# Optimization experiments

Measured on AMD Instinct MI355X. Metric: run time of the kernel, lower is better.

Reference implementation:

```python
import jax, jax.numpy as jnp
import numpy as np

B, L, C_IN = 32, 244, 128
F_NUM, KS = 64, 5
HID = 512
SA_DIV = 3
F3 = F_NUM * 3
D_SA = F3 // SA_DIV  # must equal F_NUM (sa_div==3) for the view in SelfAttention


def setup_inputs() -> dict:
    key = jax.random.key(0)
    ks = jax.random.split(key, 16)

    def rn(k, shape, fan_in):
        return jax.random.normal(k, shape, dtype=jnp.float32) * float(np.sqrt(2.0 / fan_in))

    return {
        "x": jax.random.normal(ks[0], (B, L, C_IN), dtype=jnp.float32),
        "conv1_w": rn(ks[1], (F_NUM, 1, KS, 1), KS),
        "conv1_b": jnp.zeros((F_NUM,), jnp.float32),
        "conv2_w": rn(ks[2], (F_NUM, F_NUM, KS, 1), F_NUM * KS),
        "conv2_b": jnp.zeros((F_NUM,), jnp.float32),
        "conv3_w": rn(ks[3], (F_NUM, F_NUM, KS, 1), F_NUM * KS),
        "conv3_b": jnp.zeros((F_NUM,), jnp.float32),
        "conv4_w": rn(ks[4], (F_NUM, F_NUM, KS, 1), F_NUM * KS),
        "conv4_b": jnp.zeros((F_NUM,), jnp.float32),
        "wq": rn(ks[5], (D_SA, F3), F3),
        "wk": rn(ks[6], (D_SA, F3), F3),
        "wv": rn(ks[7], (D_SA, F3), F3),
        "wv1": rn(ks[8], (D_SA, F3), F3),
        "gamma": jnp.full((1,), 0.1, jnp.float32),
        "gru_wih": rn(ks[9], (3 * HID, F_NUM * C_IN), F_NUM * C_IN),
        "gru_whh": rn(ks[10], (3 * HID, HID), HID),
        "gru_bih": jnp.zeros((3 * HID,), jnp.float32),
        "gru_bhh": jnp.zeros((3 * HID,), jnp.float32),
        "fc_w": rn(ks[11], (1, HID), HID),
        "fc_b": jnp.zeros((1,), jnp.float32),
    }


def _conv2d(x, w, b):
    y = jax.lax.conv_general_dilated(
        x, w, window_strides=(1, 1), padding="VALID",
        dimension_numbers=("NCHW", "OIHW", "NCHW"))
    return y + b[None, :, None, None]


def reference(x, conv1_w, conv1_b, conv2_w, conv2_b, conv3_w, conv3_b, conv4_w, conv4_b,
              wq, wk, wv, wv1, gamma, gru_wih, gru_whh, gru_bih, gru_bhh, fc_w, fc_b):
    # conv stack: (B,1,L,C) -> (B,F,L',C), time dim shrinks by 4*(KS-1)
    h = x[:, None, :, :]
    h = jax.nn.relu(_conv2d(h, conv1_w, conv1_b))
    h = jax.nn.relu(_conv2d(h, conv2_w, conv2_b))
    h = jax.nn.relu(_conv2d(h, conv3_w, conv3_b))
    h = jax.nn.relu(_conv2d(h, conv4_w, conv4_b))
    Bn, Fn, Lp, Cn = h.shape
    step = int(np.ceil(Lp / 3))
    # static slice starts; last slice is x[:, :, -3:, :] (matches torch loop)
    starts = np.minimum(np.arange(step) * 3, Lp - 3)
    idx = starts[:, None] + np.arange(3)                               # (S,3)
    xs = h[:, :, idx, :]                                               # (B,F,S,3,C)
    xs = xs.transpose(0, 2, 1, 3, 4).reshape(Bn, step, Fn * 3, Cn)     # (B,S,F3,C)
    # batched SelfAttention (1x1 conv1d == matmul over channel dim)
    f = jnp.einsum("df,bsfc->bsdc", wq, xs)
    g = jnp.einsum("df,bsfc->bsdc", wk, xs)
    v = jnp.einsum("df,bsfc->bsdc", wv, xs)
    v1 = jnp.einsum("df,bsfc->bsdc", wv1, xs)
    # torch: softmax(bmm(f^T, g), dim=1) -> softmax over first C axis
    beta = jax.nn.softmax(jnp.einsum("bsdc,bsdk->bsck", f, g), axis=-2)
    o = gamma[0] * jnp.einsum("bsdc,bsck->bsdk", v, beta) + v1         # (B,S,F,C)
    seq = o.transpose(1, 0, 2, 3).reshape(step, Bn, Fn * Cn)           # (S,B,F*C)
    # single-layer GRU (PyTorch gate order r,z,n), seq-first
    xg = jnp.einsum("sbi,gi->sbg", seq, gru_wih) + gru_bih             # (S,B,3H)

    def gru_step(hprev, xg_t):
        hg = hprev @ gru_whh.T + gru_bhh
        xr, xz, xn = jnp.split(xg_t, 3, axis=-1)
        hr, hz, hn = jnp.split(hg, 3, axis=-1)
        r = jax.nn.sigmoid(xr + hr)
        z = jax.nn.sigmoid(xz + hz)
        n = jnp.tanh(xn + r * hn)
        hnew = (1.0 - z) * n + z * hprev
        return hnew, hnew

    h0 = jnp.zeros((Bn, HID), seq.dtype)
    _, outs = jax.lax.scan(gru_step, h0, xg)                            # (S,B,H)
    # temporal attention pooling over the time axis (axis 0)
    att = jnp.einsum("sbh,h->sb", outs, fc_w[0]) + fc_b[0]
    w_att = jax.nn.softmax(att, axis=0)[:, :, None]
    return jnp.sum(w_att * outs, axis=0)                                # (B,H)
```

## Files before the change

kernel.cpp:

```cpp
#include <hip/hip_runtime.h>
#include <math.h>


typedef __attribute__((ext_vector_type(8))) short short8;
typedef __attribute__((ext_vector_type(4))) float f32x4;

#define XG_STRIDE 3735552ull

__device__ inline float sigm(float x){ return 1.f/(1.f+__expf(-x)); }
__device__ inline unsigned short f2bf(float f){
    unsigned int u = __float_as_uint(f);
    u = (u + 0x7FFFu + ((u >> 16) & 1u)) >> 16;
    return (unsigned short)u;
}
__device__ inline float bf2f(unsigned short h){
    return __uint_as_float(((unsigned int)h) << 16);
}
__device__ inline int xcd_chunked(int orig, int nwg){
    int q = nwg >> 3, r = nwg & 7;
    int xcd = orig & 7, i = orig >> 3;
    return (xcd < r ? xcd*(q+1) : r*(q+1) + (xcd-r)*q) + i;
}

__global__ __launch_bounds__(256) void conv1_k(const float* __restrict__ x,
        unsigned short* __restrict__ out_h, unsigned short* __restrict__ out_l,
        const float* __restrict__ w1, const float* __restrict__ b1, int b_base)
{
    __shared__ float w1s[320];
    __shared__ float b1s[64];
    int t = threadIdx.x;
    for (int idx = t; idx < 320; idx += 256) w1s[idx] = w1[idx];
    if (t < 64)  b1s[t] = b1[t];
    __syncthreads();
    int i = blockIdx.x*256 + t;
    int c = i & 127; int t2 = i >> 7;
    int l = t2 % 240; int b = t2 / 240;
    const float* xp = x + ((size_t)(b_base + b)*244 + l)*128 + c;
    float xv[5];
    #pragma unroll
    for (int k=0;k<5;++k) xv[k] = xp[k*128];
    unsigned short* oh = out_h + (size_t)i*64;
    unsigned short* ol = out_l + (size_t)i*64;
    #pragma unroll
    for (int f8=0; f8<8; ++f8){
        unsigned short rh[8], rl[8];
        #pragma unroll
        for (int j=0;j<8;++j){
            int f = f8*8 + j;
            float a = b1s[f];
            #pragma unroll
            for (int k=0;k<5;++k) a += w1s[f*5+k]*xv[k];
            a = a > 0.f ? a : 0.f;
            unsigned short hi = f2bf(a);
            rh[j] = hi;
            rl[j] = f2bf(a - bf2f(hi));
        }
        *(short8*)(oh + f8*8) = *(short8*)rh;
        *(short8*)(ol + f8*8) = *(short8*)rl;
    }
}

__global__ __launch_bounds__(256) void repack_convw_k(const float* __restrict__ w2,
        const float* __restrict__ w3, const float* __restrict__ w4,
        unsigned short* __restrict__ wbf_h, unsigned short* __restrict__ wbf_l)
{
    int idx = blockIdx.x*256 + threadIdx.x;
    int fi = idx & 63; int t2 = idx >> 6;
    int fo = t2 & 63;  int t3 = t2 >> 6;
    int k = t3 % 5;    int layer = t3 / 5;
    const float* ws_ = (layer==0)? w2 : (layer==1)? w3 : w4;
    float v = ws_[(fo*64 + fi)*5 + k];
    unsigned short hi = f2bf(v);
    wbf_h[idx] = hi;
    wbf_l[idx] = f2bf(v - bf2f(hi));
}

__global__ __launch_bounds__(256) void conv_mfma_s(
        const unsigned short* __restrict__ in_h, const unsigned short* __restrict__ in_l,
        unsigned short* __restrict__ out_h, unsigned short* __restrict__ out_l,
        const unsigned short* __restrict__ wk_h, const unsigned short* __restrict__ wk_l,
        const float* __restrict__ bias, int Lin, int Lout)
{
    __shared__ __align__(16) unsigned short Abh[64*72], Abl[64*72];
    __shared__ __align__(16) unsigned short Wbh[64*72], Wbl[64*72];
    int nblk = gridDim.x;
    int lin = xcd_chunked(blockIdx.x, nblk);
    int ch = lin & 1; int rest = lin >> 1;
    int l = rest % Lout; int b = rest / Lout;

    int t = threadIdx.x;
    int lane = t & 63, w = t >> 6;
    int lr = lane & 15, lh = lane >> 4;
    f32x4 acc[4];
    #pragma unroll
    for (int nf=0;nf<4;++nf) acc[nf] = (f32x4)0.f;

    const size_t ib = ((size_t)b*Lin + l)*8192 + (size_t)ch*4096;
    for (int k=0;k<5;++k){
        __syncthreads();
        #pragma unroll
        for (int i=0;i<2;++i){
            int idx = i*256 + t; int row = idx>>3, c8 = idx&7;
            *(short8*)&Abh[row*72 + c8*8] = *(const short8*)(in_h + ib + (size_t)k*8192 + idx*8);
            *(short8*)&Abl[row*72 + c8*8] = *(const short8*)(in_l + ib + (size_t)k*8192 + idx*8);
        }
        #pragma unroll
        for (int i=0;i<2;++i){
            int idx = i*256 + t; int row = idx>>3, c8 = idx&7;
            *(short8*)&Wbh[row*72 + c8*8] = *(const short8*)(wk_h + k*4096 + idx*8);
            *(short8*)&Wbl[row*72 + c8*8] = *(const short8*)(wk_l + k*4096 + idx*8);
        }
        __syncthreads();
        #pragma unroll
        for (int kk=0;kk<2;++kk){
            short8 ah, al, bh[4], blo[4];
            ah = *(const short8*)&Abh[(w*16+lr)*72 + kk*32 + lh*8];
            al = *(const short8*)&Abl[(w*16+lr)*72 + kk*32 + lh*8];
            #pragma unroll
            for (int nf=0;nf<4;++nf){
                bh[nf]  = *(const short8*)&Wbh[(nf*16+lr)*72 + kk*32 + lh*8];
                blo[nf] = *(const short8*)&Wbl[(nf*16+lr)*72 + kk*32 + lh*8];
            }
            #pragma unroll
            for (int nf=0;nf<4;++nf){
                acc[nf] = __builtin_amdgcn_mfma_f32_16x16x32_bf16(ah, bh[nf],  acc[nf], 0,0,0);
                acc[nf] = __builtin_amdgcn_mfma_f32_16x16x32_bf16(ah, blo[nf], acc[nf], 0,0,0);
                acc[nf] = __builtin_amdgcn_mfma_f32_16x16x32_bf16(al, bh[nf],  acc[nf], 0,0,0);
            }
        }
    }
    const size_t ob = ((size_t)b*Lout + l)*8192;
    #pragma unroll
    for (int nf=0;nf<4;++nf){
        int fo = nf*16 + lr;
        float bv = bias[fo];
        #pragma unroll
        for (int q=0;q<4;++q){
            int c = ch*64 + w*16 + lh*4 + q;
            float v = acc[nf][q] + bv;
            v = v > 0.f ? v : 0.f;
            unsigned short hi = f2bf(v);
            out_h[ob + c*64 + fo] = hi;
            out_l[ob + c*64 + fo] = f2bf(v - bf2f(hi));
        }
    }
}

__global__ __launch_bounds__(256) void repack_wrep_k(const float* __restrict__ wq,
        const float* __restrict__ wk, const float* __restrict__ wv,
        const float* __restrict__ wv1,
        unsigned short* __restrict__ wr_h, unsigned short* __restrict__ wr_l)
{
    int idx = blockIdx.x*256 + threadIdx.x;
    int ko = idx % 192; int md = idx / 192;
    int m = md >> 6, d = md & 63;
    int jj = ko >> 6, f = ko & 63;
    const float* src = (m==0)? wq : (m==1)? wk : (m==2)? wv : wv1;
    float v = src[d*192 + f*3 + jj];
    unsigned short hi = f2bf(v);
    wr_h[idx] = hi;
    wr_l[idx] = f2bf(v - bf2f(hi));
}

__global__ __launch_bounds__(256) void project_mfma_s(
        const unsigned short* __restrict__ h_h, const unsigned short* __restrict__ h_l,
        const unsigned short* __restrict__ wr_h, const unsigned short* __restrict__ wr_l,
        float* __restrict__ Fo, float* __restrict__ Go,
        float* __restrict__ Vo, float* __restrict__ V1o)
{
    __shared__ __align__(16) unsigned short Abh[64*72], Abl[64*72];
    __shared__ __align__(16) unsigned short Bbh[64*72], Bbl[64*72];
    int nblk = gridDim.x;
    int lin = xcd_chunked(blockIdx.x, nblk);
    int z = lin & 7; int rest = lin >> 3;
    int s = rest % 76; int bl = rest / 76;
    int mz = z >> 1, mh = z & 1;

    int t = threadIdx.x;
    int lane = t & 63, w = t >> 6;
    int wm = w >> 1, wn = w & 1;
    int lr = lane & 15, lh = lane >> 4;
    f32x4 acc[2][2];
    #pragma unroll
    for (int mf=0;mf<2;++mf)
        #pragma unroll
        for (int nf=0;nf<2;++nf) acc[mf][nf] = (f32x4)0.f;

    for (int jj=0;jj<3;++jj){
        __syncthreads();
        const size_t ao_ = ((size_t)bl*228 + 3*s + jj)*8192 + (size_t)mh*4096;
        #pragma unroll
        for (int i=0;i<2;++i){
            int idx = i*256 + t; int row = idx>>3, c8 = idx&7;
            *(short8*)&Abh[row*72 + c8*8] = *(const short8*)(h_h + ao_ + idx*8);
            *(short8*)&Abl[row*72 + c8*8] = *(const short8*)(h_l + ao_ + idx*8);
        }
        #pragma unroll
        for (int i=0;i<2;++i){
            int idx = i*256 + t; int row = idx>>3, c8 = idx&7;
            size_t wo = (size_t)(mz*64 + row)*192 + jj*64 + c8*8;
            *(short8*)&Bbh[row*72 + c8*8] = *(const short8*)(wr_h + wo);
            *(short8*)&Bbl[row*72 + c8*8] = *(const short8*)(wr_l + wo);
        }
        __syncthreads();
        #pragma unroll
        for (int kk=0;kk<2;++kk){
            short8 ah[2], al[2], bh[2], blo[2];
            #pragma unroll
            for (int mf=0;mf<2;++mf){
                ah[mf] = *(const short8*)&Abh[(wm*32+mf*16+lr)*72 + kk*32 + lh*8];
                al[mf] = *(const short8*)&Abl[(wm*32+mf*16+lr)*72 + kk*32 + lh*8];
            }
            #pragma unroll
            for (int nf=0;nf<2;++nf){
                bh[nf]  = *(const short8*)&Bbh[(wn*32+nf*16+lr)*72 + kk*32 + lh*8];
                blo[nf] = *(const short8*)&Bbl[(wn*32+nf*16+lr)*72 + kk*32 + lh*8];
            }
            #pragma unroll
            for (int mf=0;mf<2;++mf)
                #pragma unroll
                for (int nf=0;nf<2;++nf){
                    acc[mf][nf] = __builtin_amdgcn_mfma_f32_16x16x32_bf16(ah[mf], bh[nf],  acc[mf][nf], 0,0,0);
                    acc[mf][nf] = __builtin_amdgcn_mfma_f32_16x16x32_bf16(ah[mf], blo[nf], acc[mf][nf], 0,0,0);
                    acc[mf][nf] = __builtin_amdgcn_mfma_f32_16x16x32_bf16(al[mf], bh[nf],  acc[mf][nf], 0,0,0);
                }
        }
    }
    float* dst = (mz==0)? Fo : (mz==1)? Go : (mz==2)? Vo : V1o;
    size_t bs = (size_t)bl*76 + s;
    #pragma unroll
    for (int mf=0;mf<2;++mf)
        #pragma unroll
        for (int nf=0;nf<2;++nf){
            int d = wn*32 + nf*16 + lr;
            int c0 = mh*64 + wm*32 + mf*16 + lh*4;
            *(f32x4*)&dst[(bs*64 + d)*128 + c0] = acc[mf][nf];
        }
}

__global__ __launch_bounds__(256) void attend_k(const float* __restrict__ Fg,
        const float* __restrict__ Gg, const float* __restrict__ Vg,
        const float* __restrict__ V1g, const float* __restrict__ gamma,
        unsigned short* __restrict__ seq_bf, int b_base)
{
    __shared__ float sm[16384];
    int t = threadIdx.x;
    int s = blockIdx.x, bl = blockIdx.y;
    size_t base = ((size_t)bl*76 + s)*8192;
    for (int i=t; i<8192; i+=256) sm[i]      = Fg[base+i];
    for (int i=t; i<8192; i+=256) sm[8192+i] = Gg[base+i];
    __syncthreads();

    int k = t & 127, ch = t >> 7;
    float sc[64];
    #pragma unroll
    for (int j=0;j<64;++j) sc[j]=0.f;
    for (int d=0; d<64; ++d){
        float gk = sm[8192 + d*128 + k];
        #pragma unroll
        for (int cj=0; cj<16; ++cj){
            float4 f4 = *(const float4*)&sm[d*128 + ch*64 + cj*4];
            sc[cj*4+0] += f4.x*gk; sc[cj*4+1] += f4.y*gk;
            sc[cj*4+2] += f4.z*gk; sc[cj*4+3] += f4.w*gk;
        }
    }
    __syncthreads();
    float m = -1e30f;
    #pragma unroll
    for (int j=0;j<64;++j) m = fmaxf(m, sc[j]);
    sm[t] = m;
    for (int i=t; i<8192; i+=256) sm[8192+i] = Vg[base+i];
    __syncthreads();
    m = fmaxf(sm[k], sm[128+k]);
    float lsum = 0.f;
    #pragma unroll
    for (int j=0;j<64;++j){ sc[j] = __expf(sc[j]-m); lsum += sc[j]; }
    __syncthreads();
    sm[t] = lsum;
    __syncthreads();
    float rinv = 1.f/(sm[k] + sm[128+k]);
    #pragma unroll
    for (int j=0;j<64;++j) sc[j] *= rinv;
    __syncthreads();

    if (ch == 0){
        #pragma unroll
        for (int j=0;j<64;++j) sm[j*128 + k] = sc[j];
    }
    __syncthreads();

    int k2 = t & 31, dq = t >> 5;
    float ao[8][4];
    #pragma unroll
    for (int j=0;j<8;++j)
        #pragma unroll
        for (int mm=0;mm<4;++mm) ao[j][mm]=0.f;

    for (int c2=0; c2<64; ++c2){
        float bv0 = sm[c2*128 + k2],    bv1 = sm[c2*128 + k2+32];
        float bv2 = sm[c2*128 + k2+64], bv3 = sm[c2*128 + k2+96];
        #pragma unroll
        for (int j=0;j<8;++j){
            float v = sm[8192 + (dq*8+j)*128 + c2];
            ao[j][0]+=v*bv0; ao[j][1]+=v*bv1; ao[j][2]+=v*bv2; ao[j][3]+=v*bv3;
        }
    }
    __syncthreads();
    if (ch == 1){
        #pragma unroll
        for (int j=0;j<64;++j) sm[j*128 + k] = sc[j];
    }
    __syncthreads();
    for (int c2=64; c2<128; ++c2){
        float bv0 = sm[(c2-64)*128 + k2],    bv1 = sm[(c2-64)*128 + k2+32];
        float bv2 = sm[(c2-64)*128 + k2+64], bv3 = sm[(c2-64)*128 + k2+96];
        #pragma unroll
        for (int j=0;j<8;++j){
            float v = sm[8192 + (dq*8+j)*128 + c2];
            ao[j][0]+=v*bv0; ao[j][1]+=v*bv1; ao[j][2]+=v*bv2; ao[j][3]+=v*bv3;
        }
    }

    float gm = gamma[0];
    size_t sbase = (size_t)(s*32 + b_base + bl)*8192;
    #pragma unroll
    for (int j=0;j<8;++j){
        int d = dq*8+j;
        #pragma unroll
        for (int mm=0;mm<4;++mm){
            int kk = k2 + 32*mm;
            float val = gm*ao[j][mm] + V1g[base + (size_t)d*128 + kk];
            seq_bf[sbase + (size_t)d*128 + kk] = f2bf(val);
        }
    }
}

__global__ __launch_bounds__(256) void conv_wih_bf16(const float* __restrict__ w,
        unsigned short* __restrict__ o)
{
    int i = (blockIdx.x*256 + threadIdx.x)*4;
    float4 v = *(const float4*)&w[i];
    ushort4 r;
    r.x = f2bf(v.x); r.y = f2bf(v.y); r.z = f2bf(v.z); r.w = f2bf(v.w);
    *(ushort4*)&o[i] = r;
}

__global__ __launch_bounds__(512) void gemm_xg_mfma(const unsigned short* __restrict__ A,
        const unsigned short* __restrict__ Bw, const float* __restrict__ bih,
        float* __restrict__ out, int nsplit)
{
    __shared__ float AsF[128*36];
    __shared__ float BsF[128*36];
    int nwg = 228*nsplit;
    int wgid = xcd_chunked(blockIdx.x, nwg);
    int kz = wgid / 228;
    int r2 = wgid % 228;
    int n0 = (r2 % 12) * 128, m0 = (r2 / 12) * 128;
    int klen = 8192 / nsplit;
    int kbase = kz * klen;
    int nkt = klen >> 6;

    int t = threadIdx.x;
    int w = t >> 6;
    int wm = w >> 1, wn = w & 1;
    int lane = t & 63, lr = lane & 15, lh = lane >> 4;

    f32x4 acc[2][4];
    #pragma unroll
    for (int mi=0;mi<2;++mi)
        #pragma unroll
        for (int ni=0;ni<4;++ni) acc[mi][ni] = (f32x4)0.f;

    float4 ra[2], rb[2];
    #pragma unroll
    for (int i=0;i<2;++i){
        int idx = i*512 + t; int row = idx>>3, seg = idx&7;
        ra[i] = *(const float4*)(A  + (size_t)(m0 + row)*8192 + kbase + seg*8);
        rb[i] = *(const float4*)(Bw + (size_t)(n0 + row)*8192 + kbase + seg*8);
    }
    for (int kt=0; kt<nkt; ++kt){
        __syncthreads();
        #pragma unroll
        for (int i=0;i<2;++i){
            int idx = i*512 + t; int row = idx>>3, seg = idx&7;
            *(float4*)&AsF[row*36 + seg*4] = ra[i];
            *(float4*)&BsF[row*36 + seg*4] = rb[i];
        }
        __syncthreads();
        if (kt < nkt-1){
            int k0 = kbase + (kt+1)*64;
            #pragma unroll
            for (int i=0;i<2;++i){
                int idx = i*512 + t; int row = idx>>3, seg = idx&7;
                ra[i] = *(const float4*)(A  + (size_t)(m0 + row)*8192 + k0 + seg*8);
                rb[i] = *(const float4*)(Bw + (size_t)(n0 + row)*8192 + k0 + seg*8);
            }
        }
        #pragma unroll
        for (int kk=0;kk<2;++kk){
            short8 af[2], bf_[4];
            #pragma unroll
            for (int mi=0;mi<2;++mi)
                af[mi] = *(short8*)&AsF[(wm*32 + mi*16 + lr)*36 + kk*16 + lh*4];
            #pragma unroll
            for (int ni=0;ni<4;++ni)
                bf_[ni] = *(short8*)&BsF[(wn*64 + ni*16 + lr)*36 + kk*16 + lh*4];
            #pragma unroll
            for (int mi=0;mi<2;++mi)
                #pragma unroll
                for (int ni=0;ni<4;++ni)
                    acc[mi][ni] = __builtin_amdgcn_mfma_f32_16x16x32_bf16(
                                      bf_[ni], af[mi], acc[mi][ni], 0, 0, 0);
        }
    }
    float* op = out + (size_t)kz*XG_STRIDE;
    #pragma unroll
    for (int ni=0;ni<4;++ni){
        int nbase = n0 + wn*64 + ni*16 + lh*4;
        float4 bi4 = (kz == 0) ? *(const float4*)&bih[nbase]
                               : make_float4(0.f,0.f,0.f,0.f);
        #pragma unroll
        for (int mi=0;mi<2;++mi){
            int m = m0 + wm*32 + mi*16 + lr;
            float4 o;
            o.x = acc[mi][ni][0] + bi4.x;
            o.y = acc[mi][ni][1] + bi4.y;
            o.z = acc[mi][ni][2] + bi4.z;
            o.w = acc[mi][ni][3] + bi4.w;
            *(float4*)&op[(size_t)m*1536 + nbase] = o;
        }
    }
}

__global__ __launch_bounds__(256) void build_whhp_k(const float* __restrict__ whh,
        float4* __restrict__ whh_p)
{
    int idx = blockIdx.x*256 + threadIdx.x;
    int i = idx >> 9, j = idx & 511;
    float4 o;
    o.x = whh[(size_t)j*512 + i];
    o.y = whh[(size_t)(512+j)*512 + i];
    o.z = whh[(size_t)(1024+j)*512 + i];
    o.w = 0.f;
    whh_p[idx] = o;
}

__global__ __launch_bounds__(1024) void gru_step_k(const float4* __restrict__ whh_p,
        const float* __restrict__ xg, const float* __restrict__ bhh,
        float* __restrict__ outs, int s, int nsplit)
{
    __shared__ float hl[2048];
    __shared__ float red[4][4][64][3];
    int t = threadIdx.x;
    int jc = blockIdx.x & 7, bq = blockIdx.x >> 3;
    for (int idx=t; idx<2048; idx+=1024)
        hl[idx] = outs[(size_t)s*16384 + (size_t)(bq*4 + (idx>>9))*512 + (idx&511)];
    __syncthreads();
    int jl = t & 63, bl = (t >> 6) & 3, iq = t >> 8;
    int j = jc*64 + jl;
    float a0=0.f,a1=0.f,a2=0.f;
    const float4* wp = whh_p + (size_t)(iq*128)*512 + j;
    const float* hb = hl + bl*512 + iq*128;
    #pragma unroll 4
    for (int i=0;i<128;++i){
        float4 w4 = wp[(size_t)i*512];
        float hv = hb[i];
        a0 += w4.x*hv; a1 += w4.y*hv; a2 += w4.z*hv;
    }
    red[iq][bl][jl][0] = a0; red[iq][bl][jl][1] = a1; red[iq][bl][jl][2] = a2;
    __syncthreads();
    if (t < 256){
        int jl2 = t & 63, bl2 = t >> 6;
        int j2 = jc*64 + jl2, b = bq*4 + bl2;
        float hr=0.f, hz=0.f, hn=0.f;
        #pragma unroll
        for (int q=0;q<4;++q){
            hr += red[q][bl2][jl2][0];
            hz += red[q][bl2][jl2][1];
            hn += red[q][bl2][jl2][2];
        }
        size_t xi = (size_t)(s*32 + b)*1536 + j2;
        float xr = xg[xi], xz = xg[xi+512], xn = xg[xi+1024];
        #pragma unroll 1
        for (int q2=1; q2<nsplit; ++q2){
            xr += xg[xi + (size_t)q2*XG_STRIDE];
            xz += xg[xi + 512 + (size_t)q2*XG_STRIDE];
            xn += xg[xi + 1024 + (size_t)q2*XG_STRIDE];
        }
        hr += bhh[j2]; hz += bhh[512+j2]; hn += bhh[1024+j2];
        float r = sigm(xr+hr), z = sigm(xz+hz);
        float n = tanhf(xn + r*hn);
        float hp = hl[bl2*512 + j2];
        float hnew = (1.f - z)*n + z*hp;
        outs[(size_t)(s+1)*16384 + (size_t)b*512 + j2] = hnew;
    }
}

__global__ __launch_bounds__(256) void pool_k(const float* __restrict__ outs,
        const float* __restrict__ fcw, const float* __restrict__ fcb,
        float* __restrict__ out)
{
    __shared__ float att[80], watt[128];
    int b = blockIdx.x, t = threadIdx.x;
    int w = t >> 6, lane = t & 63;
    for (int s = w; s < 76; s += 4){
        float acc = 0.f;
        const float* op = outs + (size_t)(s+1)*16384 + (size_t)b*512;
        #pragma unroll
        for (int hh = 0; hh < 512; hh += 64) acc += op[hh+lane]*fcw[hh+lane];
        #pragma unroll
        for (int off=32; off; off>>=1) acc += __shfl_down(acc, off);
        if (lane==0) att[s] = acc + fcb[0];
    }
    __syncthreads();
    if (t < 64){
        float a0 = (t<76)? att[t] : -1e30f;
        float a1 = (t+64<76)? att[t+64] : -1e30f;
        float m = fmaxf(a0,a1);
        #pragma unroll
        for (int off=32; off; off>>=1) m = fmaxf(m, __shfl_xor(m, off));
        float e0 = (t<76)? __expf(a0-m) : 0.f;
        float e1 = (t+64<76)? __expf(a1-m) : 0.f;
        float ssum = e0+e1;
        #pragma unroll
        for (int off=32; off; off>>=1) ssum += __shfl_xor(ssum, off);
        float ri = 1.f/ssum;
        watt[t] = e0*ri;
        watt[t+64] = e1*ri;
    }
    __syncthreads();
    for (int h = t; h < 512; h += 256){
        float acc=0.f;
        for (int s=0;s<76;++s) acc += watt[s]*outs[(size_t)(s+1)*16384 + (size_t)b*512 + h];
        out[(size_t)b*512 + h] = acc;
    }
}

extern "C" void kernel_launch(void* const* d_in, const int* in_sizes, int n_in,
                              void* d_out, int out_size, void* d_ws, size_t ws_size,
                              hipStream_t stream)
{
    const float* x   = (const float*)d_in[0];
    const float* w1  = (const float*)d_in[1];  const float* b1  = (const float*)d_in[2];
    const float* w2  = (const float*)d_in[3];  const float* b2  = (const float*)d_in[4];
    const float* w3  = (const float*)d_in[5];  const float* b3  = (const float*)d_in[6];
    const float* w4  = (const float*)d_in[7];  const float* b4  = (const float*)d_in[8];
    const float* wq  = (const float*)d_in[9];  const float* wk  = (const float*)d_in[10];
    const float* wv  = (const float*)d_in[11]; const float* wv1 = (const float*)d_in[12];
    const float* gamma = (const float*)d_in[13];
    const float* wih = (const float*)d_in[14]; const float* whh = (const float*)d_in[15];
    const float* bih = (const float*)d_in[16]; const float* bhh = (const float*)d_in[17];
    const float* fcw = (const float*)d_in[18]; const float* fcb = (const float*)d_in[19];

    int nb = 2, ns = 1;
    {
        auto need = [](int nb_, int ns_)->size_t{
            return ((size_t)nb_*4521984ull + 16117760ull
                    + (size_t)(ns_-1)*3735552ull)*4ull + 4096ull;
        };
        if      (ws_size >= need(8,4)){ nb = 8; ns = 4; }
        else if (ws_size >= need(8,2)){ nb = 8; ns = 2; }
        else if (ws_size >= need(4,2)){ nb = 4; ns = 2; }
        else if (ws_size >= need(2,2)){ nb = 2; ns = 2; }
    }

    float* ws = (float*)d_ws;
    size_t off = 0;
    size_t szAh = (size_t)nb*983040ull;
    size_t szBh = (size_t)nb*966656ull;
    size_t szP  = (size_t)nb*622592ull;
    unsigned short* bufAh = (unsigned short*)(ws + off); off += szAh;
    unsigned short* bufAl = (unsigned short*)(ws + off); off += szAh;
    unsigned short* bufBh = (unsigned short*)(ws + off); off += szBh;
    unsigned short* bufBl = (unsigned short*)(ws + off); off += szBh;
    float* V1b = ws + off; off += szP;
    unsigned short* seq_bf = (unsigned short*)(ws + off); off += 9961472ull;
    float* xg   = ws + off; off += (size_t)ns*XG_STRIDE;
    float* outs = ws + off; off += 77ull*16384;
    float4* whh_p = (float4*)(ws + off); off += 1048576ull;
    unsigned short* wbf_h = (unsigned short*)(ws + off); off += 30720ull;
    unsigned short* wbf_l = (unsigned short*)(ws + off); off += 30720ull;
    unsigned short* wr_h  = (unsigned short*)(ws + off); off += 24576ull;
    unsigned short* wr_l  = (unsigned short*)(ws + off); off += 24576ull;

    float* Fb = (float*)bufAh;
    float* Gb = Fb + szP;
    float* Vb = Fb + 2*szP;
    unsigned short* wih_bf = bufAh;

    repack_convw_k<<<240, 256, 0, stream>>>(w2, w3, w4, wbf_h, wbf_l);
    repack_wrep_k<<<192, 256, 0, stream>>>(wq, wk, wv, wv1, wr_h, wr_l);
    build_whhp_k<<<1024, 256, 0, stream>>>(whh, whh_p);
    hipMemsetAsync(outs, 0, 16384*sizeof(float), stream);

    int nchunks = 32 / nb;
    for (int chunk=0; chunk<nchunks; ++chunk){
        int b_base = chunk*nb;
        conv1_k<<<nb*120, 256, 0, stream>>>(x, bufAh, bufAl, w1, b1, b_base);
        conv_mfma_s<<<236*nb*2, 256, 0, stream>>>(bufAh, bufAl, bufBh, bufBl,
                                                  wbf_h, wbf_l, b2, 240, 236);
        conv_mfma_s<<<232*nb*2, 256, 0, stream>>>(bufBh, bufBl, bufAh, bufAl,
                                                  wbf_h+20480, wbf_l+20480, b3, 236, 232);
        conv_mfma_s<<<228*nb*2, 256, 0, stream>>>(bufAh, bufAl, bufBh, bufBl,
                                                  wbf_h+40960, wbf_l+40960, b4, 232, 228);
        project_mfma_s<<<76*nb*8, 256, 0, stream>>>(bufBh, bufBl, wr_h, wr_l,
                                                    Fb, Gb, Vb, V1b);
        attend_k<<<dim3(76,nb), 256, 0, stream>>>(Fb, Gb, Vb, V1b, gamma, seq_bf, b_base);
    }
    conv_wih_bf16<<<12288, 256, 0, stream>>>(wih, wih_bf);
    gemm_xg_mfma<<<228*ns, 512, 0, stream>>>(seq_bf, wih_bf, bih, xg, ns);
    for (int s=0; s<76; ++s)
        gru_step_k<<<64, 1024, 0, stream>>>(whh_p, xg, bhh, outs, s, ns);
    pool_k<<<32, 256, 0, stream>>>(outs, fcw, fcb, (float*)d_out);
}
```

Before: 2.998 ms.

## Fuse GRU time steps into one persistent cooperative kernel with grid sync

Replaces 76 separate per-step GRU kernel launches with a single cooperative kernel that loops over time steps and uses grid-wide synchronization between steps. The initial hidden state is zeroed in-kernel, so the memset goes away. The ns=4 split configuration is dropped, and the xg accumulation is specialized for nsplit<=2. This targets launch overhead per step, in exchange for the cost of a grid barrier and a dependence on cooperative launch support.

```diff
diff --git a/kernel.cpp b/kernel.cpp
--- a/kernel.cpp
+++ b/kernel.cpp
@@ -1,5 +1,8 @@
 #include <hip/hip_runtime.h>
+#include <hip/hip_cooperative_groups.h>
 #include <math.h>
+
+namespace cg = cooperative_groups;
 
 
 typedef __attribute__((ext_vector_type(8))) short short8;
@@ -445,54 +448,60 @@
     whh_p[idx] = o;
 }
 
-__global__ __launch_bounds__(1024) void gru_step_k(const float4* __restrict__ whh_p,
+__global__ __launch_bounds__(1024) void gru_all_k(const float4* __restrict__ whh_p,
         const float* __restrict__ xg, const float* __restrict__ bhh,
-        float* __restrict__ outs, int s, int nsplit)
-{
+        float* __restrict__ outs, int nsplit)
+{
+    cg::grid_group grid = cg::this_grid();
     __shared__ float hl[2048];
     __shared__ float red[4][4][64][3];
     int t = threadIdx.x;
     int jc = blockIdx.x & 7, bq = blockIdx.x >> 3;
-    for (int idx=t; idx<2048; idx+=1024)
-        hl[idx] = outs[(size_t)s*16384 + (size_t)(bq*4 + (idx>>9))*512 + (idx&511)];
-    __syncthreads();
     int jl = t & 63, bl = (t >> 6) & 3, iq = t >> 8;
     int j = jc*64 + jl;
-    float a0=0.f,a1=0.f,a2=0.f;
-    const float4* wp = whh_p + (size_t)(iq*128)*512 + j;
-    const float* hb = hl + bl*512 + iq*128;
-    #pragma unroll 4
-    for (int i=0;i<128;++i){
-        float4 w4 = wp[(size_t)i*512];
-        float hv = hb[i];
-        a0 += w4.x*hv; a1 += w4.y*hv; a2 += w4.z*hv;
-    }
-    red[iq][bl][jl][0] = a0; red[iq][bl][jl][1] = a1; red[iq][bl][jl][2] = a2;
-    __syncthreads();
-    if (t < 256){
-        int jl2 = t & 63, bl2 = t >> 6;
-        int j2 = jc*64 + jl2, b = bq*4 + bl2;
-        float hr=0.f, hz=0.f, hn=0.f;
-        #pragma unroll
-        for (int q=0;q<4;++q){
-            hr += red[q][bl2][jl2][0];
-            hz += red[q][bl2][jl2][1];
-            hn += red[q][bl2][jl2][2];
-        }
-        size_t xi = (size_t)(s*32 + b)*1536 + j2;
-        float xr = xg[xi], xz = xg[xi+512], xn = xg[xi+1024];
-        #pragma unroll 1
-        for (int q2=1; q2<nsplit; ++q2){
-            xr += xg[xi + (size_t)q2*XG_STRIDE];
-            xz += xg[xi + 512 + (size_t)q2*XG_STRIDE];
-            xn += xg[xi + 1024 + (size_t)q2*XG_STRIDE];
-        }
-        hr += bhh[j2]; hz += bhh[512+j2]; hn += bhh[1024+j2];
-        float r = sigm(xr+hr), z = sigm(xz+hz);
-        float n = tanhf(xn + r*hn);
-        float hp = hl[bl2*512 + j2];
-        float hnew = (1.f - z)*n + z*hp;
-        outs[(size_t)(s+1)*16384 + (size_t)b*512 + j2] = hnew;
+    const float4* wp0 = whh_p + (size_t)(iq*128)*512 + j;
+
+    for (int s=0; s<76; ++s){
+        for (int idx=t; idx<2048; idx+=1024)
+            hl[idx] = (s == 0) ? 0.f
+                : outs[(size_t)s*16384 + (size_t)(bq*4 + (idx>>9))*512 + (idx&511)];
+        __syncthreads();
+        float a0=0.f,a1=0.f,a2=0.f;
+        const float* hb = hl + bl*512 + iq*128;
+        #pragma unroll 4
+        for (int i=0;i<128;++i){
+            float4 w4 = wp0[(size_t)i*512];
+            float hv = hb[i];
+            a0 += w4.x*hv; a1 += w4.y*hv; a2 += w4.z*hv;
+        }
+        red[iq][bl][jl][0] = a0; red[iq][bl][jl][1] = a1; red[iq][bl][jl][2] = a2;
+        __syncthreads();
+        if (t < 256){
+            int jl2 = t & 63, bl2 = t >> 6;
+            int j2 = jc*64 + jl2, b = bq*4 + bl2;
+            float hr=0.f, hz=0.f, hn=0.f;
+            #pragma unroll
+            for (int q=0;q<4;++q){
+                hr += red[q][bl2][jl2][0];
+                hz += red[q][bl2][jl2][1];
+                hn += red[q][bl2][jl2][2];
+            }
+            size_t xi = (size_t)(s*32 + b)*1536 + j2;
+            float xr = xg[xi], xz = xg[xi+512], xn = xg[xi+1024];
+            if (nsplit == 2){
+                xr += xg[xi + XG_STRIDE];
+                xz += xg[xi + 512 + XG_STRIDE];
+                xn += xg[xi + 1024 + XG_STRIDE];
+            }
+            hr += bhh[j2]; hz += bhh[512+j2]; hn += bhh[1024+j2];
+            float r = sigm(xr+hr), z = sigm(xz+hz);
+            float n = tanhf(xn + r*hn);
+            float hp = hl[bl2*512 + j2];
+            float hnew = (1.f - z)*n + z*hp;
+            outs[(size_t)(s+1)*16384 + (size_t)b*512 + j2] = hnew;
+        }
+        __threadfence();
+        grid.sync();
     }
 }
 
@@ -558,8 +567,7 @@
             return ((size_t)nb_*4521984ull + 16117760ull
                     + (size_t)(ns_-1)*3735552ull)*4ull + 4096ull;
         };
-        if      (ws_size >= need(8,4)){ nb = 8; ns = 4; }
-        else if (ws_size >= need(8,2)){ nb = 8; ns = 2; }
+        if      (ws_size >= need(8,2)){ nb = 8; ns = 2; }
         else if (ws_size >= need(4,2)){ nb = 4; ns = 2; }
         else if (ws_size >= need(2,2)){ nb = 2; ns = 2; }
     }
@@ -591,7 +599,6 @@
     repack_convw_k<<<240, 256, 0, stream>>>(w2, w3, w4, wbf_h, wbf_l);
     repack_wrep_k<<<192, 256, 0, stream>>>(wq, wk, wv, wv1, wr_h, wr_l);
     build_whhp_k<<<1024, 256, 0, stream>>>(whh, whh_p);
-    hipMemsetAsync(outs, 0, 16384*sizeof(float), stream);
 
     int nchunks = 32 / nb;
     for (int chunk=0; chunk<nchunks; ++chunk){
@@ -609,7 +616,12 @@
     }
     conv_wih_bf16<<<12288, 256, 0, stream>>>(wih, wih_bf);
     gemm_xg_mfma<<<228*ns, 512, 0, stream>>>(seq_bf, wih_bf, bih, xg, ns);
-    for (int s=0; s<76; ++s)
-        gru_step_k<<<64, 1024, 0, stream>>>(whh_p, xg, bhh, outs, s, ns);
+
+    {
+        void* gargs[] = { (void*)&whh_p, (void*)&xg, (void*)&bhh,
+                          (void*)&outs, (void*)&ns };
+        hipLaunchCooperativeKernel(reinterpret_cast<void*>(gru_all_k),
+                                   dim3(64), dim3(1024), gargs, 0, stream);
+    }
     pool_k<<<32, 256, 0, stream>>>(outs, fcw, fcb, (float*)d_out);
 }
```

After: 4.676 ms. 56.0% more time.
